# Performance work log

Measured on AMD Instinct MI355X. Metric: run time of the kernel, lower is better.

Reference implementation:

```python
import jax, jax.numpy as jnp
import numpy as np

B, N, C = 16, 1024, 768
H = 12
HD = C // H
MLP = 4 * C
EPS = 1e-5  # torch nn.LayerNorm default
LS_INIT = 1e-5


def _ln(x, g, b):
    mu = jnp.mean(x, axis=-1, keepdims=True)
    var = jnp.var(x, axis=-1, keepdims=True)
    return (x - mu) * jax.lax.rsqrt(var + EPS) * g + b


def setup_inputs() -> dict:
    key = jax.random.key(0)
    ks = jax.random.split(key, 8)
    s = 0.02
    return {
        "x": jax.random.normal(ks[0], (B, N, C), dtype=jnp.float32),
        "w_qkv": jax.random.normal(ks[1], (C, 3 * C), dtype=jnp.float32) * s,
        "w_proj": jax.random.normal(ks[2], (C, C), dtype=jnp.float32) * s,
        "b_proj": jnp.zeros((C,), jnp.float32),
        "ln1_g": jnp.ones((C,), jnp.float32),
        "ln1_b": jnp.zeros((C,), jnp.float32),
        "ln2_g": jnp.ones((C,), jnp.float32),
        "ln2_b": jnp.zeros((C,), jnp.float32),
        "ls1_g": jnp.full((C,), LS_INIT, jnp.float32),
        "ls2_g": jnp.full((C,), LS_INIT, jnp.float32),
        "w_fc1": jax.random.normal(ks[3], (C, MLP), dtype=jnp.float32) * s,
        "b_fc1": jnp.zeros((MLP,), jnp.float32),
        "w_fc2": jax.random.normal(ks[4], (MLP, C), dtype=jnp.float32) * s,
        "b_fc2": jnp.zeros((C,), jnp.float32),
    }


def reference(x, w_qkv, w_proj, b_proj, ln1_g, ln1_b, ln2_g, ln2_b,
              ls1_g, ls2_g, w_fc1, b_fc1, w_fc2, b_fc2):
    scale = HD ** -0.5
    # ---- attention branch (pre-norm) ----
    h = x
    y = _ln(x, ln1_g, ln1_b)
    qkv = (y @ w_qkv).reshape(B, N, 3, H, HD)
    q, k, v = (jnp.moveaxis(qkv, 2, 0)[i].transpose(0, 2, 1, 3) for i in range(3))  # [B,H,N,HD]
    attn = jnp.einsum("bhnd,bhmd->bhnm", q * scale, k)
    attn = attn - jnp.max(attn, axis=-1, keepdims=True)  # explicit max-subtract as in source
    attn = jax.nn.softmax(attn, axis=-1)
    o = jnp.einsum("bhnm,bhmd->bhnd", attn, v).transpose(0, 2, 1, 3).reshape(B, N, C)
    o = o @ w_proj + b_proj
    x = h + o * ls1_g  # LayerScale (fp32)
    # ---- MLP branch ----
    h = x
    y = _ln(x, ln2_g, ln2_b)
    y = jax.nn.gelu(y @ w_fc1 + b_fc1, approximate=False)
    y = y @ w_fc2 + b_fc2
    x = h + y * ls2_g
    return x  # weights=None since vis=False
```

## Files before the change

kernel.cpp:

```cpp
#include <hip/hip_runtime.h>
#include <cstdint>
#include <cstddef>

typedef __bf16 bf16;
typedef __bf16 bf16x4 __attribute__((ext_vector_type(4)));
typedef __bf16 bf16x8 __attribute__((ext_vector_type(8)));
typedef _Float16 f16;
typedef _Float16 f16x2 __attribute__((ext_vector_type(2)));
typedef _Float16 f16x4 __attribute__((ext_vector_type(4)));
typedef _Float16 f16x8 __attribute__((ext_vector_type(8)));
typedef float  f32x4  __attribute__((ext_vector_type(4)));
typedef float  f32x16 __attribute__((ext_vector_type(16)));
typedef int    i32x4  __attribute__((ext_vector_type(4)));
typedef int    i32x8  __attribute__((ext_vector_type(8)));
typedef unsigned char u8;

#define B_   16
#define N_   1024
#define C_   768
#define H_   12
#define HD_  64
#define M_   (B_*N_)
#define MLP_ 3072
#define QKVN 2304
#define WSCALE 64.0f
#define WINV  (1.0f/64.0f)
#define CEXP_ 0.18033688f

__device__ __forceinline__ void gll16(const void* g, void* l) {
  __builtin_amdgcn_global_load_lds((const __attribute__((address_space(1))) void*)g,
                                   (__attribute__((address_space(3))) void*)l,
                                   16, 0, 0);
}

template <int N>
__device__ __forceinline__ void wait_vm() {
  if constexpr (N == 0)      asm volatile("s_waitcnt vmcnt(0)" ::: "memory");
  else if constexpr (N == 3) asm volatile("s_waitcnt vmcnt(3)" ::: "memory");
  else                       asm volatile("s_waitcnt vmcnt(4)" ::: "memory");
}

__device__ __forceinline__ float fast_exp2(float x) { return __builtin_amdgcn_exp2f(x); }
__device__ __forceinline__ float fast_rcp(float x)  { return __builtin_amdgcn_rcpf(x); }

__device__ __forceinline__ f16x2 cvt_pk_f16(float a, float b) {
  return __builtin_bit_cast(f16x2, __builtin_amdgcn_cvt_pkrtz(a, b));
}

__device__ __forceinline__ u8 to_fp8(float a) {
  return (u8)(__builtin_amdgcn_cvt_pk_fp8_f32(a, a, 0, false) & 0xff);
}
__device__ __forceinline__ int to_fp8x4(float v0, float v1, float v2, float v3) {
  int p = __builtin_amdgcn_cvt_pk_fp8_f32(v0, v1, 0, false);
  p = __builtin_amdgcn_cvt_pk_fp8_f32(v2, v3, p, true);
  return p;
}

#define T_QKV  1728
#define T_PROJ 2304
#define T_FC1  4608
#define T_FC2  6912
#define T_ALL  6912

__device__ __forceinline__ void tc_tile(const float* __restrict__ w, u8* __restrict__ wt,
                                        int K, int N, int t, int tid) {
  __shared__ float tile[32][33];
  int tiles_n = N >> 5;
  int n0 = (t % tiles_n) * 32, k0 = (t / tiles_n) * 32;
  int tx = tid & 31, ty = tid >> 5;
  #pragma unroll
  for (int i = 0; i < 32; i += 8)
    tile[ty + i][tx] = w[(size_t)(k0 + ty + i) * N + n0 + tx];
  __syncthreads();
  #pragma unroll
  for (int i = 0; i < 32; i += 8)
    wt[(size_t)(n0 + ty + i) * K + k0 + tx] = to_fp8(tile[tx][ty + i] * WSCALE);
}

__global__ __launch_bounds__(256)
void prep_kernel(const float* __restrict__ x,
                 const float* __restrict__ w_qkv, const float* __restrict__ w_proj,
                 const float* __restrict__ w_fc1, const float* __restrict__ w_fc2,
                 const float* __restrict__ g, const float* __restrict__ bta,
                 u8* __restrict__ wqkvT, u8* __restrict__ wprojT,
                 u8* __restrict__ wfc1T, u8* __restrict__ wfc2T,
                 u8* __restrict__ y) {
  int bid = blockIdx.x, tid = threadIdx.x;
  if (bid < T_ALL) {
    if (bid < T_QKV)       tc_tile(w_qkv,  wqkvT,  C_,   QKVN, bid,          tid);
    else if (bid < T_PROJ) tc_tile(w_proj, wprojT, C_,   C_,   bid - T_QKV,  tid);
    else if (bid < T_FC1)  tc_tile(w_fc1,  wfc1T,  C_,   MLP_, bid - T_PROJ, tid);
    else                   tc_tile(w_fc2,  wfc2T,  MLP_, C_,   bid - T_FC1,  tid);
    return;
  }
  int row = bid - T_ALL;
  const float* xr = x + (size_t)row * C_;
  float v0 = xr[tid], v1 = xr[tid + 256], v2 = xr[tid + 512];
  float s  = v0 + v1 + v2;
  float sq = v0 * v0 + v1 * v1 + v2 * v2;
  #pragma unroll
  for (int off = 32; off > 0; off >>= 1) {
    s  += __shfl_xor(s,  off);
    sq += __shfl_xor(sq, off);
  }
  __shared__ float red[8];
  int wave = tid >> 6, lane = tid & 63;
  if (lane == 0) { red[wave] = s; red[4 + wave] = sq; }
  __syncthreads();
  s  = red[0] + red[1] + red[2] + red[3];
  sq = red[4] + red[5] + red[6] + red[7];
  float mean = s * (1.0f / C_);
  float var  = sq * (1.0f / C_) - mean * mean;
  float rstd = rsqrtf(var + 1e-5f);
  u8* yr = y + (size_t)row * C_;
  yr[tid]       = to_fp8((v0 - mean) * rstd * g[tid]       + bta[tid]);
  yr[tid + 256] = to_fp8((v1 - mean) * rstd * g[tid + 256] + bta[tid + 256]);
  yr[tid + 512] = to_fp8((v2 - mean) * rstd * g[tid + 512] + bta[tid + 512]);
}

__global__ __launch_bounds__(256)
void ln_cast_kernel(const float* __restrict__ x, const float* __restrict__ g,
                    const float* __restrict__ bta, u8* __restrict__ y) {
  int row = blockIdx.x;
  int tid = threadIdx.x;
  const float* xr = x + (size_t)row * C_;
  float v0 = xr[tid], v1 = xr[tid + 256], v2 = xr[tid + 512];
  float s  = v0 + v1 + v2;
  float sq = v0 * v0 + v1 * v1 + v2 * v2;
  #pragma unroll
  for (int off = 32; off > 0; off >>= 1) {
    s  += __shfl_xor(s,  off);
    sq += __shfl_xor(sq, off);
  }
  __shared__ float red[8];
  int wave = tid >> 6, lane = tid & 63;
  if (lane == 0) { red[wave] = s; red[4 + wave] = sq; }
  __syncthreads();
  s  = red[0] + red[1] + red[2] + red[3];
  sq = red[4] + red[5] + red[6] + red[7];
  float mean = s * (1.0f / C_);
  float var  = sq * (1.0f / C_) - mean * mean;
  float rstd = rsqrtf(var + 1e-5f);
  u8* yr = y + (size_t)row * C_;
  yr[tid]       = to_fp8((v0 - mean) * rstd * g[tid]       + bta[tid]);
  yr[tid + 256] = to_fp8((v1 - mean) * rstd * g[tid + 256] + bta[tid + 256]);
  yr[tid + 512] = to_fp8((v2 - mean) * rstd * g[tid + 512] + bta[tid + 512]);
}

template <int EPI, int BN_>
__global__ __launch_bounds__(512, 2)
void gemm_bt(const u8* __restrict__ A, const u8* __restrict__ Bt,
             void* __restrict__ outp, const float* __restrict__ bias,
             const float* __restrict__ ls, const float* __restrict__ resid,
             int M, int N, int K, int nb) {
  constexpr int BM = 256, BK = 64;
  constexpr int NJ  = BN_ / 128;
  constexpr int NBL = BN_ / 128;
  constexpr int TL  = 2 + NBL;
  __shared__ __align__(16) u8 As[3][BM * BK];
  __shared__ __align__(16) u8 Bs[3][BN_ * BK];
  int tid  = threadIdx.x;
  int lane = tid & 63, wave = tid >> 6;
  int h32 = lane >> 5, r5 = lane & 31;
  int bid = blockIdx.x;
  int xcd = bid & 7, seq = bid >> 3;
  int mi = xcd + 8 * (seq / nb), ni = seq % nb;
  int m0 = mi * BM, n0 = ni * BN_;
  int wm = (wave >> 2) * 128, wn = (wave & 3) * (BN_ / 4);

  int iters = K >> 6;
  int skew  = (ni * iters) / nb;

  const u8* ag[2]; const u8* bg[NBL];
  #pragma unroll
  for (int s = 0; s < 2; s++) {
    int u = tid + s * 512;
    int r = u >> 2, g = (u & 3) ^ ((r >> 1) & 3);
    ag[s] = A + (size_t)(m0 + r) * K + g * 16;
  }
  #pragma unroll
  for (int s = 0; s < NBL; s++) {
    int u = tid + s * 512;
    int r = u >> 2, g = (u & 3) ^ ((r >> 1) & 3);
    bg[s] = Bt + (size_t)(n0 + r) * K + g * 16;
  }
  int sw  = (r5 >> 1) & 3;
  int go0 = ((2 * h32 + 0) ^ sw) * 16;
  int go1 = ((2 * h32 + 1) ^ sw) * 16;

  f32x16 acc[4][NJ];
  #pragma unroll
  for (int i = 0; i < 4; i++)
    #pragma unroll
    for (int j = 0; j < NJ; j++)
      #pragma unroll
      for (int rg = 0; rg < 16; rg++) acc[i][j][rg] = 0.f;

  int k0 = skew;
  int k1 = (skew + 1 == iters) ? 0 : skew + 1;
  {
    int kn = k0 * BK;
    gll16(ag[0] + kn, &As[0][0] + tid * 16);
    gll16(ag[1] + kn, &As[0][0] + 8192 + tid * 16);
    gll16(bg[0] + kn, &Bs[0][0] + tid * 16);
    if constexpr (NBL == 2) gll16(bg[1] + kn, &Bs[0][0] + 8192 + tid * 16);
    kn = k1 * BK;
    gll16(ag[0] + kn, &As[1][0] + tid * 16);
    gll16(ag[1] + kn, &As[1][0] + 8192 + tid * 16);
    gll16(bg[0] + kn, &Bs[1][0] + tid * 16);
    if constexpr (NBL == 2) gll16(bg[1] + kn, &Bs[1][0] + 8192 + tid * 16);
  }
  wait_vm<TL>();
  __builtin_amdgcn_s_barrier();
  int kiss = (k1 + 1 == iters) ? 0 : k1 + 1;

  int buf_c = 0;
  for (int t = 0; t < iters; t++) {
    if (t + 2 < iters) {
      int bi = (buf_c == 0) ? 2 : buf_c - 1;
      int kn = kiss * BK;
      gll16(ag[0] + kn, &As[bi][0] + tid * 16);
      gll16(ag[1] + kn, &As[bi][0] + 8192 + tid * 16);
      gll16(bg[0] + kn, &Bs[bi][0] + tid * 16);
      if constexpr (NBL == 2) gll16(bg[1] + kn, &Bs[bi][0] + 8192 + tid * 16);
      kiss = (kiss + 1 == iters) ? 0 : kiss + 1;
    }
    i32x8 af[4], bfr[NJ];
    #pragma unroll
    for (int i = 0; i < 4; i++) {
      const u8* pa = &As[buf_c][0] + (wm + i * 32 + r5) * 64;
      i32x4 lo = *(const i32x4*)(pa + go0);
      i32x4 hi = *(const i32x4*)(pa + go1);
      af[i] = __builtin_shufflevector(lo, hi, 0, 1, 2, 3, 4, 5, 6, 7);
    }
    #pragma unroll
    for (int j = 0; j < NJ; j++) {
      const u8* pb = &Bs[buf_c][0] + (wn + j * 32 + r5) * 64;
      i32x4 lo = *(const i32x4*)(pb + go0);
      i32x4 hi = *(const i32x4*)(pb + go1);
      bfr[j] = __builtin_shufflevector(lo, hi, 0, 1, 2, 3, 4, 5, 6, 7);
    }
    __builtin_amdgcn_s_setprio(1);
    #pragma unroll
    for (int i = 0; i < 4; i++)
      #pragma unroll
      for (int j = 0; j < NJ; j++)
        acc[i][j] = __builtin_amdgcn_mfma_scale_f32_32x32x64_f8f6f4(
            af[i], bfr[j], acc[i][j], 0, 0, 0, 0x7f7f7f7f, 0, 0x7f7f7f7f);
    __builtin_amdgcn_s_setprio(0);
    if (t + 1 < iters) {
      if (t + 2 < iters) wait_vm<TL>();
      else               wait_vm<0>();
      __builtin_amdgcn_s_barrier();
    }
    buf_c = (buf_c == 2) ? 0 : buf_c + 1;
  }

  #pragma unroll
  for (int i = 0; i < 4; i++) {
    int rowb = m0 + wm + i * 32 + h32 * 4;
    #pragma unroll
    for (int j = 0; j < NJ; j++) {
      int col = n0 + wn + j * 32 + r5;
      float bias_c = (EPI == 0) ? 0.f : bias[col];
      float ls_c   = (EPI == 1 || EPI == 3) ? ls[col] : 0.f;
      float gz_v = -2.45546696f * WINV;
      float gz_b = -2.45546696f * bias_c;
      float sc0 = (EPI == 0) ? ((col < C_) ? (WINV * CEXP_) : WINV) : WINV;
      #pragma unroll
      for (int rg = 0; rg < 16; rg++) {
        float v = acc[i][j][rg];
        int row = rowb + (rg & 3) + 8 * (rg >> 2);
        size_t idx = (size_t)row * N + col;
        if constexpr (EPI == 0) {
          ((bf16*)outp)[idx] = (bf16)(v * sc0);
        } else if constexpr (EPI == 1) {
          float t = fmaf(v, WINV, bias_c);
          ((float*)outp)[idx] = fmaf(t, ls_c, resid[idx]);
        } else if constexpr (EPI == 2) {
          float t  = fmaf(v, WINV, bias_c);
          float zn = fmaf(v, gz_v, gz_b);
          float gv = t * fast_rcp(1.0f + fast_exp2(zn));
          ((u8*)outp)[idx] = to_fp8(gv);
        } else {
          float t = fmaf(v, WINV, bias_c);
          ((float*)outp)[idx] = fmaf(t, ls_c, resid[idx]);
        }
      }
    }
  }
}

__global__ void transpose_v(const bf16* __restrict__ qkv, f16* __restrict__ vt) {
  __shared__ bf16 tile[32][33];
  int bh = blockIdx.z;
  int b = bh / H_, h = bh % H_;
  int n0 = blockIdx.x * 32, d0 = blockIdx.y * 32;
  int tx = threadIdx.x, ty = threadIdx.y;
  const bf16* src = qkv + (size_t)(b * N_) * QKVN + 2 * C_ + h * HD_;
  #pragma unroll
  for (int i = 0; i < 32; i += 8)
    tile[ty + i][tx] = src[(size_t)(n0 + ty + i) * QKVN + d0 + tx];
  __syncthreads();
  f16* dst = vt + (size_t)bh * HD_ * N_;
  #pragma unroll
  for (int i = 0; i < 32; i += 8)
    dst[(size_t)(d0 + ty + i) * N_ + n0 + tx] = (f16)(float)tile[tx][ty + i];
}

__global__ __launch_bounds__(256)
void attn_kernel(const bf16* __restrict__ qkv, const f16* __restrict__ vt,
                 u8* __restrict__ o) {
  constexpr int KSTR = 72;
  constexpr int VSTR = 136;
  __shared__ __align__(16) bf16 Ks[128 * KSTR];
  __shared__ __align__(16) f16  Vs[HD_ * VSTR];

  int tid = threadIdx.x, lane = tid & 63, wave = tid >> 6;
  int quad = lane >> 4, l16 = lane & 15;
  int bid = blockIdx.x;
  int xcd = bid & 7, seq = bid >> 3;
  int bh = xcd + 8 * (seq >> 3);
  int b = bh / H_, h = bh % H_;
  int qt = seq & 7;
  int q0 = qt * 128;

  bf16x8 qf[2][2];
  #pragma unroll
  for (int i = 0; i < 2; i++)
    #pragma unroll
    for (int kk = 0; kk < 2; kk++)
      qf[i][kk] = *(const bf16x8*)(qkv + (size_t)(b * N_ + q0 + wave * 32 + i * 16 + l16) * QKVN
                                   + h * HD_ + kk * 32 + quad * 8);

  const f32x4 fz = {0.f, 0.f, 0.f, 0.f};
  f32x4 oacc[2][4];
  float l_run[2];
  #pragma unroll
  for (int i = 0; i < 2; i++) {
    #pragma unroll
    for (int jd = 0; jd < 4; jd++) oacc[i][jd] = fz;
    l_run[i] = 0.f;
  }

  const bf16* kbase = qkv + (size_t)(b * N_) * QKVN + C_ + h * HD_;
  const f16*  vbase = vt + (size_t)bh * HD_ * N_;

  int kr[4], kc[4], vr[4], vc[4];
  #pragma unroll
  for (int u = 0; u < 4; u++) {
    int L = tid + u * 256;
    kr[u] = L >> 3;  kc[u] = (L & 7) * 8;
    vr[u] = L >> 4;  vc[u] = (L & 15) * 8;
  }

  bf16x8 kreg[4]; f16x8 vreg[4];
  {
    int kv = qt * 128;
    #pragma unroll
    for (int u = 0; u < 4; u++) {
      kreg[u] = *(const bf16x8*)(kbase + (size_t)(kv + kr[u]) * QKVN + kc[u]);
      vreg[u] = *(const f16x8*)(vbase + (size_t)vr[u] * N_ + kv + vc[u]);
    }
  }

  for (int t = 0; t < 8; t++) {
    __syncthreads();
    #pragma unroll
    for (int u = 0; u < 4; u++) {
      *(bf16x8*)(Ks + kr[u] * KSTR + kc[u]) = kreg[u];
      *(f16x8*)(Vs + vr[u] * VSTR + vc[u])  = vreg[u];
    }
    __syncthreads();

    if (t + 1 < 8) {
      int kv = ((t + 1 + qt) & 7) * 128;
      #pragma unroll
      for (int u = 0; u < 4; u++) {
        kreg[u] = *(const bf16x8*)(kbase + (size_t)(kv + kr[u]) * QKVN + kc[u]);
        vreg[u] = *(const f16x8*)(vbase + (size_t)vr[u] * N_ + kv + vc[u]);
      }
    }

    f32x4 sv[2][8];
    #pragma unroll
    for (int i = 0; i < 2; i++)
      #pragma unroll
      for (int kf = 0; kf < 8; kf++) sv[i][kf] = fz;
    #pragma unroll
    for (int kk = 0; kk < 2; kk++) {
      #pragma unroll
      for (int kf = 0; kf < 8; kf++) {
        bf16x8 kb = *(const bf16x8*)(Ks + (kf * 16 + l16) * KSTR + kk * 32 + quad * 8);
        sv[0][kf] = __builtin_amdgcn_mfma_f32_16x16x32_bf16(kb, qf[0][kk], sv[0][kf], 0, 0, 0);
        sv[1][kf] = __builtin_amdgcn_mfma_f32_16x16x32_bf16(kb, qf[1][kk], sv[1][kf], 0, 0, 0);
      }
    }

    f16x4 pb[2][8];
    #pragma unroll
    for (int i = 0; i < 2; i++) {
      f16x2 rs2 = {(f16)0.f, (f16)0.f};
      #pragma unroll
      for (int kf = 0; kf < 8; kf++) {
        float p0 = fast_exp2(sv[i][kf][0]);
        float p1 = fast_exp2(sv[i][kf][1]);
        float p2 = fast_exp2(sv[i][kf][2]);
        float p3 = fast_exp2(sv[i][kf][3]);
        f16x2 h0 = cvt_pk_f16(p0, p1);
        f16x2 h1 = cvt_pk_f16(p2, p3);
        pb[i][kf] = __builtin_shufflevector(h0, h1, 0, 1, 2, 3);
        rs2 += h0;
        rs2 += h1;
      }
      float rs = (float)rs2[0] + (float)rs2[1];
      rs += __shfl_xor(rs, 16);
      rs += __shfl_xor(rs, 32);
      l_run[i] += rs;
    }

    #pragma unroll
    for (int kb2 = 0; kb2 < 4; kb2++) {
      f16x8 pb32_0 = __builtin_shufflevector(pb[0][2 * kb2], pb[0][2 * kb2 + 1],
                                             0, 1, 2, 3, 4, 5, 6, 7);
      f16x8 pb32_1 = __builtin_shufflevector(pb[1][2 * kb2], pb[1][2 * kb2 + 1],
                                             0, 1, 2, 3, 4, 5, 6, 7);
      #pragma unroll
      for (int jd = 0; jd < 4; jd++) {
        const f16* vp = Vs + (jd * 16 + l16) * VSTR + kb2 * 32 + quad * 4;
        f16x4 v0 = *(const f16x4*)(vp);
        f16x4 v1 = *(const f16x4*)(vp + 16);
        f16x8 va8 = __builtin_shufflevector(v0, v1, 0, 1, 2, 3, 4, 5, 6, 7);
        oacc[0][jd] = __builtin_amdgcn_mfma_f32_16x16x32_f16(va8, pb32_0, oacc[0][jd], 0, 0, 0);
        oacc[1][jd] = __builtin_amdgcn_mfma_f32_16x16x32_f16(va8, pb32_1, oacc[1][jd], 0, 0, 0);
      }
    }
  }

  #pragma unroll
  for (int i = 0; i < 2; i++) {
    float inv = fast_rcp(l_run[i]);
    int n = q0 + wave * 32 + i * 16 + l16;
    #pragma unroll
    for (int jd = 0; jd < 4; jd++) {
      int p = to_fp8x4(oacc[i][jd][0] * inv, oacc[i][jd][1] * inv,
                       oacc[i][jd][2] * inv, oacc[i][jd][3] * inv);
      *(int*)(o + (size_t)(b * N_ + n) * C_ + h * HD_ + jd * 16 + quad * 4) = p;
    }
  }
}

#define WQKVT_OFF  0u
#define WPROJT_OFF 1769472u
#define WFC1T_OFF  2359296u
#define WFC2T_OFF  4718592u
#define Y_OFF      7077888u
#define QKV_OFF    19660800u
#define VT_OFF     95158272u
#define O_OFF      120324096u
#define X1_OFF     132907008u
#define WS_NEEDED  183238656u

extern "C" void kernel_launch(void* const* d_in, const int* in_sizes, int n_in,
                              void* d_out, int out_size, void* d_ws, size_t ws_size,
                              hipStream_t stream) {
  if (ws_size < (size_t)WS_NEEDED) return;

  const float* x      = (const float*)d_in[0];
  const float* w_qkv  = (const float*)d_in[1];
  const float* w_proj = (const float*)d_in[2];
  const float* b_proj = (const float*)d_in[3];
  const float* ln1_g  = (const float*)d_in[4];
  const float* ln1_b  = (const float*)d_in[5];
  const float* ln2_g  = (const float*)d_in[6];
  const float* ln2_b  = (const float*)d_in[7];
  const float* ls1_g  = (const float*)d_in[8];
  const float* ls2_g  = (const float*)d_in[9];
  const float* w_fc1  = (const float*)d_in[10];
  const float* b_fc1  = (const float*)d_in[11];
  const float* w_fc2  = (const float*)d_in[12];
  const float* b_fc2  = (const float*)d_in[13];

  char* ws = (char*)d_ws;
  u8*    wqkvT  = (u8*)(ws + WQKVT_OFF);
  u8*    wprojT = (u8*)(ws + WPROJT_OFF);
  u8*    wfc1T  = (u8*)(ws + WFC1T_OFF);
  u8*    wfc2T  = (u8*)(ws + WFC2T_OFF);
  u8*    y      = (u8*)(ws + Y_OFF);
  bf16*  qkv    = (bf16*)(ws + QKV_OFF);
  u8*    hbuf   = (u8*)(ws + QKV_OFF);
  f16*   vt     = (f16*)(ws + VT_OFF);
  u8*    o      = (u8*)(ws + O_OFF);
  float* x1     = (float*)(ws + X1_OFF);
  float* out    = (float*)d_out;

  prep_kernel<<<T_ALL + M_, 256, 0, stream>>>(
      x, w_qkv, w_proj, w_fc1, w_fc2, ln1_g, ln1_b,
      wqkvT, wprojT, wfc1T, wfc2T, y);

  gemm_bt<0, 256><<<(M_ / 256) * (QKVN / 256), 512, 0, stream>>>(
      y, wqkvT, qkv, nullptr, nullptr, nullptr, M_, QKVN, C_, QKVN / 256);

  dim3 tb(32, 8);
  transpose_v<<<dim3(N_ / 32, HD_ / 32, B_ * H_), tb, 0, stream>>>(qkv, vt);

  attn_kernel<<<(N_ / 128) * B_ * H_, 256, 0, stream>>>(qkv, vt, o);

  gemm_bt<1, 128><<<(M_ / 256) * (C_ / 128), 512, 0, stream>>>(
      o, wprojT, x1, b_proj, ls1_g, x, M_, C_, C_, C_ / 128);

  ln_cast_kernel<<<M_, 256, 0, stream>>>(x1, ln2_g, ln2_b, y);

  gemm_bt<2, 256><<<(M_ / 256) * (MLP_ / 256), 512, 0, stream>>>(
      y, wfc1T, hbuf, b_fc1, nullptr, nullptr, M_, MLP_, C_, MLP_ / 256);

  gemm_bt<3, 128><<<(M_ / 256) * (C_ / 128), 512, 0, stream>>>(
      hbuf, wfc2T, out, b_fc2, ls2_g, x1, M_, C_, MLP_, C_ / 128);
}
```

Before: 448.6 us.

## Fuse V transpose into QKV GEMM epilogue and double attention query tile

```diff
diff --git a/kernel.cpp b/kernel.cpp
--- a/kernel.cpp
+++ b/kernel.cpp
@@ -152,6 +152,7 @@
 void gemm_bt(const u8* __restrict__ A, const u8* __restrict__ Bt,
              void* __restrict__ outp, const float* __restrict__ bias,
              const float* __restrict__ ls, const float* __restrict__ resid,
+             f16* __restrict__ vt_out,
              int M, int N, int K, int nb) {
   constexpr int BM = 256, BK = 64;
   constexpr int NJ  = BN_ / 128;
@@ -266,49 +267,51 @@
       float ls_c   = (EPI == 1 || EPI == 3) ? ls[col] : 0.f;
       float gz_v = -2.45546696f * WINV;
       float gz_b = -2.45546696f * bias_c;
-      float sc0 = (EPI == 0) ? ((col < C_) ? (WINV * CEXP_) : WINV) : WINV;
-      #pragma unroll
-      for (int rg = 0; rg < 16; rg++) {
-        float v = acc[i][j][rg];
-        int row = rowb + (rg & 3) + 8 * (rg >> 2);
-        size_t idx = (size_t)row * N + col;
-        if constexpr (EPI == 0) {
-          ((bf16*)outp)[idx] = (bf16)(v * sc0);
-        } else if constexpr (EPI == 1) {
-          float t = fmaf(v, WINV, bias_c);
-          ((float*)outp)[idx] = fmaf(t, ls_c, resid[idx]);
-        } else if constexpr (EPI == 2) {
-          float t  = fmaf(v, WINV, bias_c);
-          float zn = fmaf(v, gz_v, gz_b);
-          float gv = t * fast_rcp(1.0f + fast_exp2(zn));
-          ((u8*)outp)[idx] = to_fp8(gv);
-        } else {
-          float t = fmaf(v, WINV, bias_c);
-          ((float*)outp)[idx] = fmaf(t, ls_c, resid[idx]);
+      if constexpr (EPI == 0) {
+        float sc0 = (col < C_) ? (WINV * CEXP_) : WINV;
+        bool isv = (n0 + wn + j * 32) >= 2 * C_;
+        #pragma unroll
+        for (int g = 0; g < 4; g++) {
+          f16x4 vv;
+          #pragma unroll
+          for (int rr = 0; rr < 4; rr++) {
+            float v = acc[i][j][4 * g + rr];
+            int row = rowb + rr + 8 * g;
+            ((bf16*)outp)[(size_t)row * N + col] = (bf16)(v * sc0);
+            vv[rr] = (f16)(v * WINV);
+          }
+          if (isv) {
+            int row0 = rowb + 8 * g;
+            int bb = row0 >> 10, nn = row0 & 1023;
+            int hh = (col - 2 * C_) >> 6, dd = (col - 2 * C_) & 63;
+            *(f16x4*)(vt_out + ((size_t)(bb * H_ + hh) * HD_ + dd) * N_ + nn) = vv;
+          }
+        }
+      } else {
+        #pragma unroll
+        for (int rg = 0; rg < 16; rg++) {
+          float v = acc[i][j][rg];
+          int row = rowb + (rg & 3) + 8 * (rg >> 2);
+          size_t idx = (size_t)row * N + col;
+          if constexpr (EPI == 1) {
+            float t = fmaf(v, WINV, bias_c);
+            ((float*)outp)[idx] = fmaf(t, ls_c, resid[idx]);
+          } else if constexpr (EPI == 2) {
+            float t  = fmaf(v, WINV, bias_c);
+            float zn = fmaf(v, gz_v, gz_b);
+            float gv = t * fast_rcp(1.0f + fast_exp2(zn));
+            ((u8*)outp)[idx] = to_fp8(gv);
+          } else {
+            float t = fmaf(v, WINV, bias_c);
+            ((float*)outp)[idx] = fmaf(t, ls_c, resid[idx]);
+          }
         }
       }
     }
   }
 }
 
-__global__ void transpose_v(const bf16* __restrict__ qkv, f16* __restrict__ vt) {
-  __shared__ bf16 tile[32][33];
-  int bh = blockIdx.z;
-  int b = bh / H_, h = bh % H_;
-  int n0 = blockIdx.x * 32, d0 = blockIdx.y * 32;
-  int tx = threadIdx.x, ty = threadIdx.y;
-  const bf16* src = qkv + (size_t)(b * N_) * QKVN + 2 * C_ + h * HD_;
-  #pragma unroll
-  for (int i = 0; i < 32; i += 8)
-    tile[ty + i][tx] = src[(size_t)(n0 + ty + i) * QKVN + d0 + tx];
-  __syncthreads();
-  f16* dst = vt + (size_t)bh * HD_ * N_;
-  #pragma unroll
-  for (int i = 0; i < 32; i += 8)
-    dst[(size_t)(d0 + ty + i) * N_ + n0 + tx] = (f16)(float)tile[tx][ty + i];
-}
-
-__global__ __launch_bounds__(256)
+__global__ __launch_bounds__(256, 3)
 void attn_kernel(const bf16* __restrict__ qkv, const f16* __restrict__ vt,
                  u8* __restrict__ o) {
   constexpr int KSTR = 72;
@@ -320,28 +323,33 @@
   int quad = lane >> 4, l16 = lane & 15;
   int bid = blockIdx.x;
   int xcd = bid & 7, seq = bid >> 3;
-  int bh = xcd + 8 * (seq >> 3);
+  int bh = xcd + 8 * (seq >> 2);
   int b = bh / H_, h = bh % H_;
-  int qt = seq & 7;
-  int q0 = qt * 128;
-
-  bf16x8 qf[2][2];
-  #pragma unroll
-  for (int i = 0; i < 2; i++)
-    #pragma unroll
-    for (int kk = 0; kk < 2; kk++)
-      qf[i][kk] = *(const bf16x8*)(qkv + (size_t)(b * N_ + q0 + wave * 32 + i * 16 + l16) * QKVN
-                                   + h * HD_ + kk * 32 + quad * 8);
+  int qt = seq & 3;
+  int q0 = qt * 256;
+
+  bf16x8 qf[2][2][2];
+  #pragma unroll
+  for (int qs = 0; qs < 2; qs++)
+    #pragma unroll
+    for (int i = 0; i < 2; i++)
+      #pragma unroll
+      for (int kk = 0; kk < 2; kk++)
+        qf[qs][i][kk] = *(const bf16x8*)(qkv
+            + (size_t)(b * N_ + q0 + qs * 128 + wave * 32 + i * 16 + l16) * QKVN
+            + h * HD_ + kk * 32 + quad * 8);
 
   const f32x4 fz = {0.f, 0.f, 0.f, 0.f};
-  f32x4 oacc[2][4];
-  float l_run[2];
-  #pragma unroll
-  for (int i = 0; i < 2; i++) {
-    #pragma unroll
-    for (int jd = 0; jd < 4; jd++) oacc[i][jd] = fz;
-    l_run[i] = 0.f;
-  }
+  f32x4 oacc[2][2][4];
+  float l_run[2][2];
+  #pragma unroll
+  for (int qs = 0; qs < 2; qs++)
+    #pragma unroll
+    for (int i = 0; i < 2; i++) {
+      #pragma unroll
+      for (int jd = 0; jd < 4; jd++) oacc[qs][i][jd] = fz;
+      l_run[qs][i] = 0.f;
+    }
 
   const bf16* kbase = qkv + (size_t)(b * N_) * QKVN + C_ + h * HD_;
   const f16*  vbase = vt + (size_t)bh * HD_ * N_;
@@ -356,7 +364,7 @@
 
   bf16x8 kreg[4]; f16x8 vreg[4];
   {
-    int kv = qt * 128;
+    int kv = (2 * qt) * 128;
     #pragma unroll
     for (int u = 0; u < 4; u++) {
       kreg[u] = *(const bf16x8*)(kbase + (size_t)(kv + kr[u]) * QKVN + kc[u]);
@@ -374,7 +382,7 @@
     __syncthreads();
 
     if (t + 1 < 8) {
-      int kv = ((t + 1 + qt) & 7) * 128;
+      int kv = ((t + 1 + 2 * qt) & 7) * 128;
       #pragma unroll
       for (int u = 0; u < 4; u++) {
         kreg[u] = *(const bf16x8*)(kbase + (size_t)(kv + kr[u]) * QKVN + kc[u]);
@@ -382,72 +390,77 @@
       }
     }
 
-    f32x4 sv[2][8];
-    #pragma unroll
-    for (int i = 0; i < 2; i++)
-      #pragma unroll
-      for (int kf = 0; kf < 8; kf++) sv[i][kf] = fz;
-    #pragma unroll
-    for (int kk = 0; kk < 2; kk++) {
-      #pragma unroll
-      for (int kf = 0; kf < 8; kf++) {
-        bf16x8 kb = *(const bf16x8*)(Ks + (kf * 16 + l16) * KSTR + kk * 32 + quad * 8);
-        sv[0][kf] = __builtin_amdgcn_mfma_f32_16x16x32_bf16(kb, qf[0][kk], sv[0][kf], 0, 0, 0);
-        sv[1][kf] = __builtin_amdgcn_mfma_f32_16x16x32_bf16(kb, qf[1][kk], sv[1][kf], 0, 0, 0);
+    #pragma unroll
+    for (int qs = 0; qs < 2; qs++) {
+      f32x4 sv[2][8];
+      #pragma unroll
+      for (int i = 0; i < 2; i++)
+        #pragma unroll
+        for (int kf = 0; kf < 8; kf++) sv[i][kf] = fz;
+      #pragma unroll
+      for (int kk = 0; kk < 2; kk++) {
+        #pragma unroll
+        for (int kf = 0; kf < 8; kf++) {
+          bf16x8 kb = *(const bf16x8*)(Ks + (kf * 16 + l16) * KSTR + kk * 32 + quad * 8);
+          sv[0][kf] = __builtin_amdgcn_mfma_f32_16x16x32_bf16(kb, qf[qs][0][kk], sv[0][kf], 0, 0, 0);
+          sv[1][kf] = __builtin_amdgcn_mfma_f32_16x16x32_bf16(kb, qf[qs][1][kk], sv[1][kf], 0, 0, 0);
+        }
       }
-    }
-
-    f16x4 pb[2][8];
+
+      f16x4 pb[2][8];
+      #pragma unroll
+      for (int i = 0; i < 2; i++) {
+        f16x2 rs2 = {(f16)0.f, (f16)0.f};
+        #pragma unroll
+        for (int kf = 0; kf < 8; kf++) {
+          float p0 = fast_exp2(sv[i][kf][0]);
+          float p1 = fast_exp2(sv[i][kf][1]);
+          float p2 = fast_exp2(sv[i][kf][2]);
+          float p3 = fast_exp2(sv[i][kf][3]);
+          f16x2 h0 = cvt_pk_f16(p0, p1);
+          f16x2 h1 = cvt_pk_f16(p2, p3);
+          pb[i][kf] = __builtin_shufflevector(h0, h1, 0, 1, 2, 3);
+          rs2 += h0;
+          rs2 += h1;
+        }
+        float rs = (float)rs2[0] + (float)rs2[1];
+        rs += __shfl_xor(rs, 16);
+        rs += __shfl_xor(rs, 32);
+        l_run[qs][i] += rs;
+      }
+
+      #pragma unroll
+      for (int kb2 = 0; kb2 < 4; kb2++) {
+        f16x8 pb32_0 = __builtin_shufflevector(pb[0][2 * kb2], pb[0][2 * kb2 + 1],
+                                               0, 1, 2, 3, 4, 5, 6, 7);
+        f16x8 pb32_1 = __builtin_shufflevector(pb[1][2 * kb2], pb[1][2 * kb2 + 1],
+                                               0, 1, 2, 3, 4, 5, 6, 7);
+        #pragma unroll
+        for (int jd = 0; jd < 4; jd++) {
+          const f16* vp = Vs + (jd * 16 + l16) * VSTR + kb2 * 32 + quad * 4;
+          f16x4 v0 = *(const f16x4*)(vp);
+          f16x4 v1 = *(const f16x4*)(vp + 16);
+          f16x8 va8 = __builtin_shufflevector(v0, v1, 0, 1, 2, 3, 4, 5, 6, 7);
+          oacc[qs][0][jd] = __builtin_amdgcn_mfma_f32_16x16x32_f16(va8, pb32_0, oacc[qs][0][jd], 0, 0, 0);
+          oacc[qs][1][jd] = __builtin_amdgcn_mfma_f32_16x16x32_f16(va8, pb32_1, oacc[qs][1][jd], 0, 0, 0);
+        }
+      }
+    }
+  }
+
+  #pragma unroll
+  for (int qs = 0; qs < 2; qs++)
     #pragma unroll
     for (int i = 0; i < 2; i++) {
-      f16x2 rs2 = {(f16)0.f, (f16)0.f};
-      #pragma unroll
-      for (int kf = 0; kf < 8; kf++) {
-        float p0 = fast_exp2(sv[i][kf][0]);
-        float p1 = fast_exp2(sv[i][kf][1]);
-        float p2 = fast_exp2(sv[i][kf][2]);
-        float p3 = fast_exp2(sv[i][kf][3]);
-        f16x2 h0 = cvt_pk_f16(p0, p1);
-        f16x2 h1 = cvt_pk_f16(p2, p3);
-        pb[i][kf] = __builtin_shufflevector(h0, h1, 0, 1, 2, 3);
-        rs2 += h0;
-        rs2 += h1;
+      float inv = fast_rcp(l_run[qs][i]);
+      int n = q0 + qs * 128 + wave * 32 + i * 16 + l16;
+      #pragma unroll
+      for (int jd = 0; jd < 4; jd++) {
+        int p = to_fp8x4(oacc[qs][i][jd][0] * inv, oacc[qs][i][jd][1] * inv,
+                         oacc[qs][i][jd][2] * inv, oacc[qs][i][jd][3] * inv);
+        *(int*)(o + (size_t)(b * N_ + n) * C_ + h * HD_ + jd * 16 + quad * 4) = p;
       }
-      float rs = (float)rs2[0] + (float)rs2[1];
-      rs += __shfl_xor(rs, 16);
-      rs += __shfl_xor(rs, 32);
-      l_run[i] += rs;
-    }
-
-    #pragma unroll
-    for (int kb2 = 0; kb2 < 4; kb2++) {
-      f16x8 pb32_0 = __builtin_shufflevector(pb[0][2 * kb2], pb[0][2 * kb2 + 1],
-                                             0, 1, 2, 3, 4, 5, 6, 7);
-      f16x8 pb32_1 = __builtin_shufflevector(pb[1][2 * kb2], pb[1][2 * kb2 + 1],
-                                             0, 1, 2, 3, 4, 5, 6, 7);
-      #pragma unroll
-      for (int jd = 0; jd < 4; jd++) {
-        const f16* vp = Vs + (jd * 16 + l16) * VSTR + kb2 * 32 + quad * 4;
-        f16x4 v0 = *(const f16x4*)(vp);
-        f16x4 v1 = *(const f16x4*)(vp + 16);
-        f16x8 va8 = __builtin_shufflevector(v0, v1, 0, 1, 2, 3, 4, 5, 6, 7);
-        oacc[0][jd] = __builtin_amdgcn_mfma_f32_16x16x32_f16(va8, pb32_0, oacc[0][jd], 0, 0, 0);
-        oacc[1][jd] = __builtin_amdgcn_mfma_f32_16x16x32_f16(va8, pb32_1, oacc[1][jd], 0, 0, 0);
-      }
-    }
-  }
-
-  #pragma unroll
-  for (int i = 0; i < 2; i++) {
-    float inv = fast_rcp(l_run[i]);
-    int n = q0 + wave * 32 + i * 16 + l16;
-    #pragma unroll
-    for (int jd = 0; jd < 4; jd++) {
-      int p = to_fp8x4(oacc[i][jd][0] * inv, oacc[i][jd][1] * inv,
-                       oacc[i][jd][2] * inv, oacc[i][jd][3] * inv);
-      *(int*)(o + (size_t)(b * N_ + n) * C_ + h * HD_ + jd * 16 + quad * 4) = p;
-    }
-  }
+    }
 }
 
 #define WQKVT_OFF  0u
@@ -499,21 +512,18 @@
       wqkvT, wprojT, wfc1T, wfc2T, y);
 
   gemm_bt<0, 256><<<(M_ / 256) * (QKVN / 256), 512, 0, stream>>>(
-      y, wqkvT, qkv, nullptr, nullptr, nullptr, M_, QKVN, C_, QKVN / 256);
-
-  dim3 tb(32, 8);
-  transpose_v<<<dim3(N_ / 32, HD_ / 32, B_ * H_), tb, 0, stream>>>(qkv, vt);
-
-  attn_kernel<<<(N_ / 128) * B_ * H_, 256, 0, stream>>>(qkv, vt, o);
+      y, wqkvT, qkv, nullptr, nullptr, nullptr, vt, M_, QKVN, C_, QKVN / 256);
+
+  attn_kernel<<<(N_ / 256) * B_ * H_, 256, 0, stream>>>(qkv, vt, o);
 
   gemm_bt<1, 128><<<(M_ / 256) * (C_ / 128), 512, 0, stream>>>(
-      o, wprojT, x1, b_proj, ls1_g, x, M_, C_, C_, C_ / 128);
+      o, wprojT, x1, b_proj, ls1_g, x, nullptr, M_, C_, C_, C_ / 128);
 
   ln_cast_kernel<<<M_, 256, 0, stream>>>(x1, ln2_g, ln2_b, y);
 
   gemm_bt<2, 256><<<(M_ / 256) * (MLP_ / 256), 512, 0, stream>>>(
-      y, wfc1T, hbuf, b_fc1, nullptr, nullptr, M_, MLP_, C_, MLP_ / 256);
+      y, wfc1T, hbuf, b_fc1, nullptr, nullptr, nullptr, M_, MLP_, C_, MLP_ / 256);
 
   gemm_bt<3, 128><<<(M_ / 256) * (C_ / 128), 512, 0, stream>>>(
-      hbuf, wfc2T, out, b_fc2, ls2_g, x1, M_, C_, MLP_, C_ / 128);
-}
+      hbuf, wfc2T, out, b_fc2, ls2_g, x1, nullptr, M_, C_, MLP_, C_ / 128);
+}
```

Measured after the change: 654.9 us. 46.0% more time.
